# Kernel optimization log

Hardware: AMD Instinct MI355X
Metric: run time of the kernel (lower is better)

The kernel has to match this reference:

```python
import jax, jax.numpy as jnp
import numpy as np

A_NUM = 9
C_NUM = 20

def setup_inputs() -> dict:
    key = jax.random.key(0)
    ks = jax.random.split(key, 12)
    B, Cin, H, W = 32, 256, 56, 56
    hidden = 256
    N, M = 64, 2048
    out_ch = 5 * A_NUM + C_NUM
    features = jax.random.normal(ks[0], (B, Cin, H, W), jnp.float32)
    w1 = jax.random.normal(ks[1], (hidden, Cin), jnp.float32) * (1.0 / np.sqrt(Cin))
    b1 = jax.random.normal(ks[2], (hidden,), jnp.float32) * 0.01
    w2 = jax.random.normal(ks[3], (out_ch, hidden), jnp.float32) * (1.0 / np.sqrt(hidden))
    b2 = jax.random.normal(ks[4], (out_ch,), jnp.float32) * 0.01
    # anchor shapes (w, h), positive sizes in grid units
    anc = 1.0 + 5.0 * jax.random.uniform(ks[5], (A_NUM, 2), jnp.float32)
    # grid of cell centers
    xs = jnp.arange(W, dtype=jnp.float32) + 0.5
    ys = jnp.arange(H, dtype=jnp.float32) + 0.5
    gx, gy = jnp.meshgrid(xs, ys, indexing='xy')  # (H, W)
    grid = jnp.broadcast_to(jnp.stack([gx, gy], axis=-1)[None], (B, H, W, 2))
    # GT boxes (x1, y1, x2, y2, cls) with x1<x2, y1<y2
    x1 = jax.random.uniform(ks[6], (B, N), jnp.float32) * (W - 9.0)
    y1 = jax.random.uniform(ks[7], (B, N), jnp.float32) * (H - 9.0)
    bw = 1.0 + 7.0 * jax.random.uniform(ks[8], (B, N), jnp.float32)
    bh = 1.0 + 7.0 * jax.random.uniform(ks[9], (B, N), jnp.float32)
    cls = jax.random.randint(ks[10], (B, N), 0, C_NUM).astype(jnp.float32)
    bboxes = jnp.stack([x1, y1, x1 + bw, y1 + bh, cls], axis=-1)
    total_anchors = B * A_NUM * H * W
    pos_anchor_idx = jax.random.randint(ks[11], (M,), 0, total_anchors, jnp.int64 if jax.config.jax_enable_x64 else jnp.int32)
    neg_anchor_idx = jax.random.randint(jax.random.fold_in(key, 99), (M,), 0, total_anchors, jnp.int64 if jax.config.jax_enable_x64 else jnp.int32)
    GT_offsets = jax.random.normal(jax.random.fold_in(key, 100), (M, 4), jnp.float32) * 0.1
    return {"features": features, "w1": w1, "b1": b1, "w2": w2, "b2": b2,
            "anc": anc, "grid": grid, "bboxes": bboxes, "GT_offsets": GT_offsets,
            "pos_anchor_idx": pos_anchor_idx, "neg_anchor_idx": neg_anchor_idx}

def _generate_anchor(anc, grid):
    # grid: (B,H,W,2), anc: (A,2) -> anchors (B,A,H,W,4) as (x1,y1,x2,y2)
    g = grid[:, None]                      # (B,1,H,W,2)
    a = anc[None, :, None, None]           # (1,A,1,1,2)
    return jnp.concatenate([g - a / 2, g + a / 2], axis=-1)

def _generate_proposal_yolo(anchors, offsets):
    ctr = (anchors[..., :2] + anchors[..., 2:]) / 2
    wh = anchors[..., 2:] - anchors[..., :2]
    new_wh = wh * jnp.exp(offsets[..., 2:])
    new_ctr = ctr + offsets[..., :2]
    return jnp.concatenate([new_ctr - new_wh / 2, new_ctr + new_wh / 2], axis=-1)

def _iou(proposals, bboxes):
    # proposals (B,A,H,W,4) -> (B,AHW,4); bboxes (B,N,5) -> iou (B,AHW,N)
    B = proposals.shape[0]
    p = proposals.reshape(B, -1, 4)[:, :, None, :]   # (B,AHW,1,4)
    g = bboxes[:, None, :, :]                        # (B,1,N,5)
    ix1 = jnp.maximum(p[..., 0], g[..., 0])
    iy1 = jnp.maximum(p[..., 1], g[..., 1])
    ix2 = jnp.minimum(p[..., 2], g[..., 2])
    iy2 = jnp.minimum(p[..., 3], g[..., 3])
    inter = jnp.clip(ix2 - ix1, 0) * jnp.clip(iy2 - iy1, 0)
    gt_area = (bboxes[:, :, 2] - bboxes[:, :, 0]) * (bboxes[:, :, 3] - bboxes[:, :, 1])
    p_area = (p[..., 2] - p[..., 0]) * (p[..., 3] - p[..., 1])
    return inter / (gt_area[:, None, :] + p_area - inter)

def reference(features, w1, b1, w2, b2, anc, grid, bboxes, GT_offsets,
              pos_anchor_idx, neg_anchor_idx):
    B, _, H, W = features.shape
    A = anc.shape[0]
    M = pos_anchor_idx.shape[0]
    # PredictionNetwork (dropout in eval = identity), 1x1 convs as einsum
    x = jnp.einsum('bchw,oc->bohw', features, w1) + b1[None, :, None, None]
    x = jax.nn.leaky_relu(x, 0.01)
    x = jnp.einsum('bchw,oc->bohw', x, w2) + b2[None, :, None, None]
    anc_data = x[:, :5 * A].reshape(B, A, 5, H, W)
    class_all = x[:, 5 * A:]                               # (B,C,H,W)
    conf_all = jax.nn.sigmoid(anc_data[:, :, 0])           # (B,A,H,W)
    offsets_all = jnp.transpose(anc_data[:, :, 1:5], (0, 1, 3, 4, 2))  # (B,A,H,W,4)
    # training extraction
    conf_flat = conf_all.reshape(-1)
    conf_scores = jnp.concatenate([conf_flat[pos_anchor_idx], conf_flat[neg_anchor_idx]])[:, None]  # (2M,1)
    offsets_pos = offsets_all.reshape(-1, 4)[pos_anchor_idx]            # (M,4)
    # class scores for positive anchors: index arithmetic over (B,A,H,W)
    bi = pos_anchor_idx // (A * H * W)
    hw = pos_anchor_idx % (H * W)
    hi, wi = hw // W, hw % W
    class_pos = class_all[bi, :, hi, wi]                                # (M,C)
    # anchors -> proposals -> IoU
    anchors = _generate_anchor(anc, grid)
    proposals = _generate_proposal_yolo(anchors, offsets_all)
    iou_mat = _iou(proposals, bboxes)                                   # (B,AHW,N)
    # YOLO SSE losses
    gt_conf = jnp.concatenate([jnp.ones((M, 1), conf_scores.dtype), jnp.zeros((M, 1), conf_scores.dtype)])
    conf_loss = jnp.sum((conf_scores - gt_conf) ** 2) / (2 * M)
    reg_loss = jnp.sum((offsets_pos - GT_offsets) ** 2) / M
    total_loss = conf_loss + reg_loss
    return total_loss, iou_mat, class_pos
```

## Files before the change

kernel.cpp:

```cpp
#include <hip/hip_runtime.h>
#include <math.h>

#define B_    32
#define CIN   256
#define HID   256
#define OC    65
#define A_    9
#define H_    56
#define W_    56
#define HW    3136
#define AHW   28224
#define NBOX  64
#define M_    2048
#define CNUM  20
#define NTILE 49

#define IOU_N ((size_t)B_ * AHW * NBOX)

#define FOFF(frag) (((frag) << 3) + ((((frag) >> 3)) << 3))

typedef _Float16 half8 __attribute__((ext_vector_type(8)));
typedef float f32x16 __attribute__((ext_vector_type(16)));
typedef float f32x4  __attribute__((ext_vector_type(4)));

__device__ __forceinline__ unsigned int pkh(float a, float b) {
    _Float16 ha = (_Float16)a, hb = (_Float16)b;
    unsigned short ua = __builtin_bit_cast(unsigned short, ha);
    unsigned short ub = __builtin_bit_cast(unsigned short, hb);
    return (unsigned int)ua | ((unsigned int)ub << 16);
}

__global__ __launch_bounds__(256) void prep_kernel(
    const float* __restrict__ w1, const float* __restrict__ w2,
    _Float16* __restrict__ w1s, _Float16* __restrict__ w2s,
    float* __restrict__ loss_ws)
{
    const int f = blockIdx.x * 256 + threadIdx.x;
    if (f < 2) loss_ws[f] = 0.f;
    {
        const int e    = f & 7;
        const int lane = (f >> 3) & 63;
        const int kc   = (f >> 9) & 15;
        const int ob   = f >> 13;
        const int row  = ob * 32 + (lane & 31);
        const int k    = kc * 16 + (lane >> 5) * 8 + e;
        w1s[f] = (_Float16)w1[row * CIN + k];
    }
    if (f < 20480) {
        const int e    = f & 7;
        const int lane = (f >> 3) & 63;
        const int ks2  = (f >> 9) & 7;
        const int rt   = f >> 12;
        const int row  = rt * 16 + (lane & 15);
        const int k    = ks2 * 32 + (lane >> 4) * 8 + e;
        w2s[f] = (row < OC) ? (_Float16)w2[row * HID + k] : (_Float16)0.f;
    }
}

__global__ __launch_bounds__(256) void conv_iou_kernel(
    const float* __restrict__ features, const _Float16* __restrict__ w1s,
    const float* __restrict__ b1, const _Float16* __restrict__ w2s,
    const float* __restrict__ b2, const float* __restrict__ anc,
    const float* __restrict__ bboxes, const int* __restrict__ pos_idx,
    const int* __restrict__ neg_idx, const float* __restrict__ gt_off,
    float* __restrict__ iou_out, float* __restrict__ cls_out,
    float* __restrict__ loss_ws)
{
    __shared__ _Float16 lds_h[18432];
    __shared__ float bias_s[HID];
    __shared__ float boxs[5 * 64];
    __shared__ float red[8];

    _Float16* featAll = lds_h;
    _Float16* hidf    = lds_h;
    float*    L       = (float*)lds_h;
    float*    x2t     = L;
    float*    ppx1    = L + 4416;
    float*    ppy1    = L + 4992;
    float*    ppx2    = L + 5568;
    float*    ppy2    = L + 6144;
    float*    pare    = L + 6720;

    const int t    = threadIdx.x;
    const int lane = t & 63;
    const int w    = t >> 6;
    const int bid  = blockIdx.x;
    const int b    = bid / NTILE;
    const int p0   = (bid - b * NTILE) * 64;
    const float* fbase = features + (size_t)b * CIN * HW + p0;

    bias_s[t] = b1[t];
    if (t < 64) {
        const float* gb = bboxes + ((size_t)b * NBOX + t) * 5;
        const float x1 = gb[0], y1 = gb[1], x2v = gb[2], y2v = gb[3];
        boxs[t] = x1; boxs[64 + t] = y1; boxs[128 + t] = x2v; boxs[192 + t] = y2v;
        boxs[256 + t] = (x2v - x1) * (y2v - y1);
    }

    const int pstage = (t & 15) * 4;
    const int kk     = (t >> 4) * 2;
    const int ksS    = kk >> 4;
    const int gS     = (kk >> 3) & 1;
    const int j0h    = kk & 7;
    const int ghalf  = lane >> 5;

#pragma unroll
    for (int hf = 0; hf < 2; ++hf) {
        float4 r0[4], r1[4];
#pragma unroll
        for (int c4 = 0; c4 < 4; ++c4) {
            const int c = hf * 4 + c4;
            r0[c4] = *(const float4*)(fbase + (size_t)(c * 32 + kk) * HW + pstage);
            r1[c4] = *(const float4*)(fbase + (size_t)(c * 32 + kk + 1) * HW + pstage);
        }
#pragma unroll
        for (int c4 = 0; c4 < 4; ++c4) {
            const int c = hf * 4 + c4;
            const float a0[4] = {r0[c4].x, r0[c4].y, r0[c4].z, r0[c4].w};
            const float a1[4] = {r1[c4].x, r1[c4].y, r1[c4].z, r1[c4].w};
#pragma unroll
            for (int e = 0; e < 4; ++e) {
                const int p     = pstage + e;
                const int lane2 = gS * 32 + (p & 31);
                const int pt    = p >> 5;
                const int frag  = c * 256 + (ksS * 2 + pt) * 64 + lane2;
                *(unsigned int*)&featAll[FOFF(frag) + j0h] = pkh(a0[e], a1[e]);
            }
        }
    }
    __syncthreads();

    f32x16 facc[2][2];
#pragma unroll
    for (int ot = 0; ot < 2; ++ot)
#pragma unroll
        for (int pt = 0; pt < 2; ++pt)
#pragma unroll
            for (int e = 0; e < 16; ++e) facc[ot][pt][e] = 0.f;

    half8 afb[2][2][2];
#pragma unroll
    for (int ks = 0; ks < 2; ++ks)
#pragma unroll
        for (int ot = 0; ot < 2; ++ot)
            afb[0][ks][ot] = *(const half8*)(w1s + ((size_t)((w * 2 + ot) * 16 + ks) * 64 + lane) * 8);

#pragma unroll
    for (int c = 0; c < 8; ++c) {
        if (c < 7) {
#pragma unroll
            for (int ks = 0; ks < 2; ++ks)
#pragma unroll
                for (int ot = 0; ot < 2; ++ot)
                    afb[(c + 1) & 1][ks][ot] =
                        *(const half8*)(w1s + ((size_t)((w * 2 + ot) * 16 + (c + 1) * 2 + ks) * 64 + lane) * 8);
        }
#pragma unroll
        for (int ks = 0; ks < 2; ++ks) {
#pragma unroll
            for (int pt = 0; pt < 2; ++pt) {
                const half8 bf = *(const half8*)&featAll[FOFF(c * 256 + (ks * 2 + pt) * 64 + lane)];
                facc[0][pt] = __builtin_amdgcn_mfma_f32_32x32x16_f16(afb[c & 1][ks][0], bf, facc[0][pt], 0, 0, 0);
                facc[1][pt] = __builtin_amdgcn_mfma_f32_32x32x16_f16(afb[c & 1][ks][1], bf, facc[1][pt], 0, 0, 0);
            }
        }
    }
    __syncthreads();

    const int col = lane & 31;
#pragma unroll
    for (int ot = 0; ot < 2; ++ot) {
        const int ks2 = w * 2 + ot;
#pragma unroll
        for (int pt = 0; pt < 2; ++pt) {
            const int pt2 = pt * 2 + (col >> 4);
            const int n15 = col & 15;
#pragma unroll
            for (int q = 0; q < 4; ++q) {
                float hv[4];
#pragma unroll
                for (int i = 0; i < 4; ++i) {
                    const int row = i + 8 * q + 4 * ghalf;
                    float v = facc[ot][pt][q * 4 + i] + bias_s[w * 64 + ot * 32 + row];
                    hv[i] = v < 0.f ? 0.01f * v : v;
                }
                const int frag = (ks2 * 4 + pt2) * 64 + (q * 16 + n15);
                *(unsigned int*)&hidf[FOFF(frag) + 4 * ghalf]     = pkh(hv[0], hv[1]);
                *(unsigned int*)&hidf[FOFF(frag) + 4 * ghalf + 2] = pkh(hv[2], hv[3]);
            }
        }
    }
    __syncthreads();

    f32x4 c2[5];
#pragma unroll
    for (int rt = 0; rt < 5; ++rt)
#pragma unroll
        for (int e = 0; e < 4; ++e) c2[rt][e] = 0.f;

    const int m16 = lane & 15;
    const int kgr = lane >> 4;
#pragma unroll 2
    for (int ks2 = 0; ks2 < 8; ++ks2) {
        const half8 bf = *(const half8*)&hidf[FOFF((ks2 * 4 + w) * 64 + lane)];
#pragma unroll
        for (int rt = 0; rt < 5; ++rt) {
            const half8 af = *(const half8*)(w2s + ((size_t)(rt * 8 + ks2) * 64 + lane) * 8);
            c2[rt] = __builtin_amdgcn_mfma_f32_16x16x32_f16(af, bf, c2[rt], 0, 0, 0);
        }
    }
    __syncthreads();

    const int pxl = w * 16 + m16;
#pragma unroll
    for (int rt = 0; rt < 5; ++rt) {
#pragma unroll
        for (int r = 0; r < 4; ++r) {
            const int o2 = rt * 16 + kgr * 4 + r;
            if (o2 < OC) x2t[pxl * 69 + o2] = c2[rt][r] + b2[o2];
        }
    }
    __syncthreads();

    for (int pi = t; pi < A_ * 64; pi += 256) {
        const int a  = pi >> 6;
        const int px = pi & 63;
        const float* xr = x2t + px * 69 + 5 * a;
        const float tx = xr[1], ty = xr[2], tw = xr[3], th = xr[4];
        const int hw = p0 + px;
        const int h  = hw / W_;
        const int wv = hw - h * W_;
        const float gx = (float)wv + 0.5f;
        const float gy = (float)h + 0.5f;
        const float nw = anc[2 * a]     * __expf(tw);
        const float nh = anc[2 * a + 1] * __expf(th);
        const float cx = gx + tx, cy = gy + ty;
        ppx1[pi] = cx - 0.5f * nw; ppy1[pi] = cy - 0.5f * nh;
        ppx2[pi] = cx + 0.5f * nw; ppy2[pi] = cy + 0.5f * nh;
        pare[pi] = nw * nh;
    }
    __syncthreads();

    const int pr = lane >> 4;
    const int j0 = (lane & 15) * 4;
    float Bx1[4], By1[4], Bx2[4], By2[4], Ba[4];
#pragma unroll
    for (int e = 0; e < 4; ++e) {
        Bx1[e] = boxs[j0 + e];       By1[e] = boxs[64 + j0 + e];
        Bx2[e] = boxs[128 + j0 + e]; By2[e] = boxs[192 + j0 + e];
        Ba[e]  = boxs[256 + j0 + e];
    }
    float* ibase = iou_out + ((size_t)b * AHW + p0) * 64;
#pragma unroll 1
    for (int a = 0; a < A_; ++a) {
#pragma unroll
        for (int q = 0; q < 4; ++q) {
            const int p = w * 16 + q * 4 + pr;
            const int i = a * 64 + p;
            const float Px1 = ppx1[i], Py1 = ppy1[i], Px2 = ppx2[i], Py2 = ppy2[i];
            const float pa = pare[i];
            f32x4 o4;
#pragma unroll
            for (int e = 0; e < 4; ++e) {
                const float iw = fminf(Px2, Bx2[e]) - fmaxf(Px1, Bx1[e]);
                const float ih = fminf(Py2, By2[e]) - fmaxf(Py1, By1[e]);
                const float inter = fmaxf(iw, 0.f) * fmaxf(ih, 0.f);
                o4[e] = inter * __builtin_amdgcn_rcpf(Ba[e] + pa - inter);
            }
            *(f32x4*)(ibase + ((size_t)a * HW + p) * 64 + j0) = o4;
        }
    }

    float csum = 0.f, rsum = 0.f;
    for (int m = t; m < M_; m += 256) {
        const int idx = pos_idx[m];
        const int bi  = idx / AHW;
        const int rr  = idx - bi * AHW;
        const int a   = rr / HW;
        const int px  = (rr - a * HW) - p0;
        if (bi == b && px >= 0 && px < 64) {
            const float* xr = x2t + px * 69;
            const float s = 1.f / (1.f + __expf(-xr[5 * a]));
            csum += (s - 1.f) * (s - 1.f);
#pragma unroll
            for (int k = 0; k < 4; ++k) {
                const float d = xr[5 * a + 1 + k] - gt_off[m * 4 + k];
                rsum += d * d;
            }
            float* co = cls_out + (size_t)m * CNUM;
#pragma unroll
            for (int c = 0; c < CNUM; ++c) co[c] = xr[45 + c];
        }
    }
    for (int m = t; m < M_; m += 256) {
        const int idx = neg_idx[m];
        const int bi  = idx / AHW;
        const int rr  = idx - bi * AHW;
        const int a   = rr / HW;
        const int px  = (rr - a * HW) - p0;
        if (bi == b && px >= 0 && px < 64) {
            const float s = 1.f / (1.f + __expf(-x2t[px * 69 + 5 * a]));
            csum += s * s;
        }
    }
#pragma unroll
    for (int off = 32; off > 0; off >>= 1) {
        csum += __shfl_down(csum, off, 64);
        rsum += __shfl_down(rsum, off, 64);
    }
    if (lane == 0) { red[w] = csum; red[4 + w] = rsum; }
    __syncthreads();
    if (t == 0) {
        const float c  = red[0] + red[1] + red[2] + red[3];
        const float rg = red[4] + red[5] + red[6] + red[7];
        if (c != 0.f || rg != 0.f) {
            atomicAdd(&loss_ws[0], c);
            atomicAdd(&loss_ws[1], rg);
        }
    }
}

__global__ void finalize_kernel(const float* __restrict__ loss_ws, float* __restrict__ out0)
{
    out0[0] = loss_ws[0] / (2.f * (float)M_) + loss_ws[1] / (float)M_;
}

extern "C" void kernel_launch(void* const* d_in, const int* in_sizes, int n_in,
                              void* d_out, int out_size, void* d_ws, size_t ws_size,
                              hipStream_t stream) {
    (void)in_sizes; (void)n_in; (void)out_size; (void)ws_size;
    const float* features = (const float*)d_in[0];
    const float* w1       = (const float*)d_in[1];
    const float* b1       = (const float*)d_in[2];
    const float* w2       = (const float*)d_in[3];
    const float* b2       = (const float*)d_in[4];
    const float* anc      = (const float*)d_in[5];
    const float* bboxes   = (const float*)d_in[7];
    const float* gt_off   = (const float*)d_in[8];
    const int*   pos_idx  = (const int*)d_in[9];
    const int*   neg_idx  = (const int*)d_in[10];
    float* out = (float*)d_out;

    char* wsb = (char*)d_ws;
    _Float16* w1s  = (_Float16*)wsb;
    _Float16* w2s  = w1s + 65536;
    float* loss_ws = (float*)(wsb + 131072 + 40960);

    prep_kernel<<<256, 256, 0, stream>>>(w1, w2, w1s, w2s, loss_ws);
    conv_iou_kernel<<<B_ * NTILE, 256, 0, stream>>>(features, w1s, b1, w2s, b2,
                                                    anc, bboxes, pos_idx, neg_idx,
                                                    gt_off, out + 1,
                                                    out + 1 + IOU_N, loss_ws);
    finalize_kernel<<<1, 1, 0, stream>>>(loss_ws, out);
}
```

Baseline: 390.2 us.

## Make proposal decode wave-local, double-buffer w2 fragment loads, fuse pos/neg loops

After: 385.9 us (median of 2 runs). Within noise of the previous version (-1.1%).

```diff
diff --git a/kernel.cpp b/kernel.cpp
--- a/kernel.cpp
+++ b/kernel.cpp
@@ -75,11 +75,6 @@
     _Float16* hidf    = lds_h;
     float*    L       = (float*)lds_h;
     float*    x2t     = L;
-    float*    ppx1    = L + 4416;
-    float*    ppy1    = L + 4992;
-    float*    ppx2    = L + 5568;
-    float*    ppy2    = L + 6144;
-    float*    pare    = L + 6720;
 
     const int t    = threadIdx.x;
     const int lane = t & 63;
@@ -88,6 +83,8 @@
     const int b    = bid / NTILE;
     const int p0   = (bid - b * NTILE) * 64;
     const float* fbase = features + (size_t)b * CIN * HW + p0;
+
+    float* WPw = L + 4416 + w * 720;
 
     bias_s[t] = b1[t];
     if (t < 64) {
@@ -200,14 +197,24 @@
 
     const int m16 = lane & 15;
     const int kgr = lane >> 4;
-#pragma unroll 2
+
+    half8 afc[2][5];
+#pragma unroll
+    for (int rt = 0; rt < 5; ++rt)
+        afc[0][rt] = *(const half8*)(w2s + ((size_t)(rt * 8) * 64 + lane) * 8);
+
+#pragma unroll
     for (int ks2 = 0; ks2 < 8; ++ks2) {
+        if (ks2 < 7) {
+#pragma unroll
+            for (int rt = 0; rt < 5; ++rt)
+                afc[(ks2 + 1) & 1][rt] =
+                    *(const half8*)(w2s + ((size_t)(rt * 8 + ks2 + 1) * 64 + lane) * 8);
+        }
         const half8 bf = *(const half8*)&hidf[FOFF((ks2 * 4 + w) * 64 + lane)];
 #pragma unroll
-        for (int rt = 0; rt < 5; ++rt) {
-            const half8 af = *(const half8*)(w2s + ((size_t)(rt * 8 + ks2) * 64 + lane) * 8);
-            c2[rt] = __builtin_amdgcn_mfma_f32_16x16x32_f16(af, bf, c2[rt], 0, 0, 0);
-        }
+        for (int rt = 0; rt < 5; ++rt)
+            c2[rt] = __builtin_amdgcn_mfma_f32_16x16x32_f16(afc[ks2 & 1][rt], bf, c2[rt], 0, 0, 0);
     }
     __syncthreads();
 
@@ -220,26 +227,28 @@
             if (o2 < OC) x2t[pxl * 69 + o2] = c2[rt][r] + b2[o2];
         }
     }
-    __syncthreads();
-
-    for (int pi = t; pi < A_ * 64; pi += 256) {
-        const int a  = pi >> 6;
-        const int px = pi & 63;
-        const float* xr = x2t + px * 69 + 5 * a;
+    asm volatile("" ::: "memory");
+
+    for (int i = lane; i < A_ * 16; i += 64) {
+        const int a  = i >> 4;
+        const int pw = i & 15;
+        const float* xr = x2t + (w * 16 + pw) * 69 + 5 * a;
         const float tx = xr[1], ty = xr[2], tw = xr[3], th = xr[4];
-        const int hw = p0 + px;
-        const int h  = hw / W_;
-        const int wv = hw - h * W_;
+        const int hwg = p0 + w * 16 + pw;
+        const int h   = hwg / W_;
+        const int wv  = hwg - h * W_;
         const float gx = (float)wv + 0.5f;
         const float gy = (float)h + 0.5f;
         const float nw = anc[2 * a]     * __expf(tw);
         const float nh = anc[2 * a + 1] * __expf(th);
         const float cx = gx + tx, cy = gy + ty;
-        ppx1[pi] = cx - 0.5f * nw; ppy1[pi] = cy - 0.5f * nh;
-        ppx2[pi] = cx + 0.5f * nw; ppy2[pi] = cy + 0.5f * nh;
-        pare[pi] = nw * nh;
-    }
-    __syncthreads();
+        WPw[i]       = cx - 0.5f * nw;
+        WPw[144 + i] = cy - 0.5f * nh;
+        WPw[288 + i] = cx + 0.5f * nw;
+        WPw[432 + i] = cy + 0.5f * nh;
+        WPw[576 + i] = nw * nh;
+    }
+    asm volatile("" ::: "memory");
 
     const int pr = lane >> 4;
     const int j0 = (lane & 15) * 4;
@@ -253,54 +262,62 @@
     float* ibase = iou_out + ((size_t)b * AHW + p0) * 64;
 #pragma unroll 1
     for (int a = 0; a < A_; ++a) {
+        float Px1[4], Py1[4], Px2[4], Py2[4], Pa[4];
 #pragma unroll
         for (int q = 0; q < 4; ++q) {
-            const int p = w * 16 + q * 4 + pr;
-            const int i = a * 64 + p;
-            const float Px1 = ppx1[i], Py1 = ppy1[i], Px2 = ppx2[i], Py2 = ppy2[i];
-            const float pa = pare[i];
+            const int idx = a * 16 + q * 4 + pr;
+            Px1[q] = WPw[idx];       Py1[q] = WPw[144 + idx];
+            Px2[q] = WPw[288 + idx]; Py2[q] = WPw[432 + idx];
+            Pa[q]  = WPw[576 + idx];
+        }
+#pragma unroll
+        for (int q = 0; q < 4; ++q) {
             f32x4 o4;
 #pragma unroll
             for (int e = 0; e < 4; ++e) {
-                const float iw = fminf(Px2, Bx2[e]) - fmaxf(Px1, Bx1[e]);
-                const float ih = fminf(Py2, By2[e]) - fmaxf(Py1, By1[e]);
+                const float iw = fminf(Px2[q], Bx2[e]) - fmaxf(Px1[q], Bx1[e]);
+                const float ih = fminf(Py2[q], By2[e]) - fmaxf(Py1[q], By1[e]);
                 const float inter = fmaxf(iw, 0.f) * fmaxf(ih, 0.f);
-                o4[e] = inter * __builtin_amdgcn_rcpf(Ba[e] + pa - inter);
-            }
-            *(f32x4*)(ibase + ((size_t)a * HW + p) * 64 + j0) = o4;
-        }
-    }
+                o4[e] = inter * __builtin_amdgcn_rcpf(Ba[e] + Pa[q] - inter);
+            }
+            *(f32x4*)(ibase + ((size_t)(a * HW) + w * 16 + q * 4 + pr) * 64 + j0) = o4;
+        }
+    }
+
+    __syncthreads();
 
     float csum = 0.f, rsum = 0.f;
     for (int m = t; m < M_; m += 256) {
-        const int idx = pos_idx[m];
-        const int bi  = idx / AHW;
-        const int rr  = idx - bi * AHW;
-        const int a   = rr / HW;
-        const int px  = (rr - a * HW) - p0;
-        if (bi == b && px >= 0 && px < 64) {
-            const float* xr = x2t + px * 69;
-            const float s = 1.f / (1.f + __expf(-xr[5 * a]));
-            csum += (s - 1.f) * (s - 1.f);
-#pragma unroll
-            for (int k = 0; k < 4; ++k) {
-                const float d = xr[5 * a + 1 + k] - gt_off[m * 4 + k];
-                rsum += d * d;
-            }
-            float* co = cls_out + (size_t)m * CNUM;
-#pragma unroll
-            for (int c = 0; c < CNUM; ++c) co[c] = xr[45 + c];
-        }
-    }
-    for (int m = t; m < M_; m += 256) {
-        const int idx = neg_idx[m];
-        const int bi  = idx / AHW;
-        const int rr  = idx - bi * AHW;
-        const int a   = rr / HW;
-        const int px  = (rr - a * HW) - p0;
-        if (bi == b && px >= 0 && px < 64) {
-            const float s = 1.f / (1.f + __expf(-x2t[px * 69 + 5 * a]));
-            csum += s * s;
+        const int ip = pos_idx[m];
+        const int in_ = neg_idx[m];
+        {
+            const int bi  = ip / AHW;
+            const int rr  = ip - bi * AHW;
+            const int a   = rr / HW;
+            const int px  = (rr - a * HW) - p0;
+            if (bi == b && px >= 0 && px < 64) {
+                const float* xr = x2t + px * 69;
+                const float s = 1.f / (1.f + __expf(-xr[5 * a]));
+                csum += (s - 1.f) * (s - 1.f);
+#pragma unroll
+                for (int k = 0; k < 4; ++k) {
+                    const float d = xr[5 * a + 1 + k] - gt_off[m * 4 + k];
+                    rsum += d * d;
+                }
+                float* co = cls_out + (size_t)m * CNUM;
+#pragma unroll
+                for (int c = 0; c < CNUM; ++c) co[c] = xr[45 + c];
+            }
+        }
+        {
+            const int bi  = in_ / AHW;
+            const int rr  = in_ - bi * AHW;
+            const int a   = rr / HW;
+            const int px  = (rr - a * HW) - p0;
+            if (bi == b && px >= 0 && px < 64) {
+                const float s = 1.f / (1.f + __expf(-x2t[px * 69 + 5 * a]));
+                csum += s * s;
+            }
         }
     }
 #pragma unroll
```
